# Performance work log

Measured on AMD Instinct MI355X. Metric: run time of the kernel, lower is better.

Reference implementation:

```python
import jax, jax.numpy as jnp
import numpy as np


def setup_inputs() -> dict:
    key = jax.random.key(0)
    ks = jax.random.split(key, 6)
    B, T, D, Dg, U = 64, 2048, 256, 256, 256
    return {
        "x": jax.random.normal(ks[0], (B, T, D), dtype=jnp.float32),
        "g": jax.random.normal(ks[1], (B, 1, Dg), dtype=jnp.float32),
        "W": jax.random.normal(ks[2], (D, U), dtype=jnp.float32) * 0.05,
        "Wg": jax.random.normal(ks[3], (Dg, U), dtype=jnp.float32) * 0.05,
        "b": jax.random.normal(ks[4], (U,), dtype=jnp.float32) * 0.05,
        "v": jax.random.normal(ks[5], (U,), dtype=jnp.float32) * 0.05,
    }


def reference(x, g, W, Wg, b, v):
    # x: [B, T, D], g: [B, 1, Dg]
    g2 = g[:, 0, :]                                  # [B, Dg]
    atten_g = (g2 @ Wg)[:, None, :]                  # [B, 1, U]
    # activation is linear (default activation=None in Keras)
    et = jnp.einsum('btd,du->btu', x, W) + atten_g + b   # [B, T, U]
    scores = jnp.einsum('btu,u->bt', et, v)          # [B, T]
    at = jax.nn.softmax(scores, axis=-1)             # softmax over sequence
    return jnp.einsum('bt,btd->bd', at, x)           # weighted sum pooling
```

## Files before the change

kernel.cpp:

```cpp
#include <hip/hip_runtime.h>

#define B 64
#define T 2048
#define D 256
#define U 256
#define NC 16
#define TC (T / NC)


__global__ __launch_bounds__(256) void k_wv(const float* __restrict__ W,
                                            const float* __restrict__ v,
                                            float* __restrict__ wv) {
    int d = threadIdx.x;
    const float4* Wr = (const float4*)(W + d * U);
    const float4* v4 = (const float4*)v;
    float acc = 0.f;
    #pragma unroll 4
    for (int u = 0; u < U / 4; ++u) {
        float4 w = Wr[u];
        float4 vv = v4[u];
        acc += w.x * vv.x + w.y * vv.y + w.z * vv.z + w.w * vv.w;
    }
    wv[d] = acc;
}

__global__ __launch_bounds__(256) void k_scores(const float* __restrict__ x,
                                                const float* __restrict__ wv,
                                                float* __restrict__ scores) {
    int lane = threadIdx.x & 63;
    int wave = threadIdx.x >> 6;
    long long rowbase = (long long)blockIdx.x * 16 + wave * 4;
    float4 w4 = ((const float4*)wv)[lane];
    #pragma unroll
    for (int i = 0; i < 4; ++i) {
        long long r = rowbase + i;
        float4 xv = ((const float4*)(x + r * D))[lane];
        float s = xv.x * w4.x + xv.y * w4.y + xv.z * w4.z + xv.w * w4.w;
        #pragma unroll
        for (int off = 32; off > 0; off >>= 1)
            s += __shfl_down(s, off, 64);
        if (lane == 0) scores[r] = s;
    }
}

__global__ __launch_bounds__(256) void k_softmax(float* __restrict__ scores) {
    int b = blockIdx.x;
    float* s = scores + (long long)b * T;
    int lane = threadIdx.x & 63, wid = threadIdx.x >> 6;
    float loc[T / 256];
    float mx = -1e30f;
    #pragma unroll
    for (int k = 0; k < T / 256; ++k) {
        loc[k] = s[threadIdx.x + k * 256];
        mx = fmaxf(mx, loc[k]);
    }
    #pragma unroll
    for (int off = 32; off > 0; off >>= 1)
        mx = fmaxf(mx, __shfl_down(mx, off, 64));
    __shared__ float sm[4];
    __shared__ float bc[2];
    if (lane == 0) sm[wid] = mx;
    __syncthreads();
    if (threadIdx.x == 0)
        bc[0] = fmaxf(fmaxf(sm[0], sm[1]), fmaxf(sm[2], sm[3]));
    __syncthreads();
    mx = bc[0];
    float sum = 0.f;
    #pragma unroll
    for (int k = 0; k < T / 256; ++k) {
        loc[k] = __expf(loc[k] - mx);
        sum += loc[k];
    }
    #pragma unroll
    for (int off = 32; off > 0; off >>= 1)
        sum += __shfl_down(sum, off, 64);
    __syncthreads();
    if (lane == 0) sm[wid] = sum;
    __syncthreads();
    if (threadIdx.x == 0)
        bc[1] = 1.f / (sm[0] + sm[1] + sm[2] + sm[3]);
    __syncthreads();
    float inv = bc[1];
    #pragma unroll
    for (int k = 0; k < T / 256; ++k)
        s[threadIdx.x + k * 256] = loc[k] * inv;
}

__global__ __launch_bounds__(256) void k_accum(const float* __restrict__ x,
                                               const float* __restrict__ p,
                                               float* __restrict__ partial) {
    int b = blockIdx.x >> 4;
    int c = blockIdx.x & (NC - 1);
    int l = threadIdx.x & 63;
    int q = threadIdx.x >> 6;
    const float4* xb = (const float4*)(x + ((long long)b * T + (long long)c * TC) * D);
    const float* pb = p + (long long)b * T + c * TC;
    float4 acc = {0.f, 0.f, 0.f, 0.f};
    for (int t = q; t < TC; t += 4) {
        float pv = pb[t];
        float4 xv = xb[(long long)t * 64 + l];
        acc.x = fmaf(pv, xv.x, acc.x);
        acc.y = fmaf(pv, xv.y, acc.y);
        acc.z = fmaf(pv, xv.z, acc.z);
        acc.w = fmaf(pv, xv.w, acc.w);
    }
    __shared__ float4 red[4][64];
    red[q][l] = acc;
    __syncthreads();
    if (q == 0) {
        float4 a0 = red[0][l], a1 = red[1][l], a2 = red[2][l], a3 = red[3][l];
        float4 r;
        r.x = a0.x + a1.x + a2.x + a3.x;
        r.y = a0.y + a1.y + a2.y + a3.y;
        r.z = a0.z + a1.z + a2.z + a3.z;
        r.w = a0.w + a1.w + a2.w + a3.w;
        ((float4*)(partial + (long long)blockIdx.x * D))[l] = r;
    }
}

__global__ __launch_bounds__(256) void k_reduce(const float* __restrict__ partial,
                                               float* __restrict__ out) {
    int b = blockIdx.x;
    int d = threadIdx.x;
    float acc = 0.f;
    #pragma unroll
    for (int c = 0; c < NC; ++c)
        acc += partial[((long long)(b * NC + c)) * D + d];
    out[(long long)b * D + d] = acc;
}

extern "C" void kernel_launch(void* const* d_in, const int* in_sizes, int n_in,
                              void* d_out, int out_size, void* d_ws, size_t ws_size,
                              hipStream_t stream) {
    const float* x = (const float*)d_in[0];
    const float* W = (const float*)d_in[2];
    const float* v = (const float*)d_in[5];
    float* ws = (float*)d_ws;
    float* wv      = ws;
    float* scores  = ws + 256;
    float* partial = ws + 256 + B * T;
    float* out = (float*)d_out;

    k_wv<<<1, 256, 0, stream>>>(W, v, wv);
    k_scores<<<(B * T) / 16, 256, 0, stream>>>(x, wv, scores);
    k_softmax<<<B, 256, 0, stream>>>(scores);
    k_accum<<<B * NC, 256, 0, stream>>>(x, scores, partial);
    k_reduce<<<B, 256, 0, stream>>>(partial, out);
}
```

Baseline: 232.1 us.

## Fuse scores, softmax and pooling into single-pass online-softmax kernel

Replaces the separate score, softmax and weighted-accumulate kernels with one kernel that computes each row's score and keeps a running max, sum and rescaled accumulator (online softmax). Per-chunk partial max, sum and output are combined in a final kernel. This reads x once instead of twice (x is 128 MiB) and removes two launches. In exchange, every row now pays two exps and a serial cross-lane reduction inside the streaming loop, which may limit how much memory traffic stays in flight.

After: 211.2 us. 1.1x faster.

```diff
diff --git a/kernel.cpp b/kernel.cpp
--- a/kernel.cpp
+++ b/kernel.cpp
@@ -7,6 +7,10 @@
 #define NC 16
 #define TC (T / NC)
 
+#define WS_WV   0
+#define WS_M    (WS_WV + 256)
+#define WS_L    (WS_M + B * NC)
+#define WS_O    (WS_L + B * NC)
 
 __global__ __launch_bounds__(256) void k_wv(const float* __restrict__ W,
                                             const float* __restrict__ v,
@@ -24,109 +28,81 @@
     wv[d] = acc;
 }
 
-__global__ __launch_bounds__(256) void k_scores(const float* __restrict__ x,
-                                                const float* __restrict__ wv,
-                                                float* __restrict__ scores) {
-    int lane = threadIdx.x & 63;
-    int wave = threadIdx.x >> 6;
-    long long rowbase = (long long)blockIdx.x * 16 + wave * 4;
-    float4 w4 = ((const float4*)wv)[lane];
-    #pragma unroll
-    for (int i = 0; i < 4; ++i) {
-        long long r = rowbase + i;
-        float4 xv = ((const float4*)(x + r * D))[lane];
-        float s = xv.x * w4.x + xv.y * w4.y + xv.z * w4.z + xv.w * w4.w;
-        #pragma unroll
-        for (int off = 32; off > 0; off >>= 1)
-            s += __shfl_down(s, off, 64);
-        if (lane == 0) scores[r] = s;
-    }
-}
-
-__global__ __launch_bounds__(256) void k_softmax(float* __restrict__ scores) {
-    int b = blockIdx.x;
-    float* s = scores + (long long)b * T;
-    int lane = threadIdx.x & 63, wid = threadIdx.x >> 6;
-    float loc[T / 256];
-    float mx = -1e30f;
-    #pragma unroll
-    for (int k = 0; k < T / 256; ++k) {
-        loc[k] = s[threadIdx.x + k * 256];
-        mx = fmaxf(mx, loc[k]);
-    }
-    #pragma unroll
-    for (int off = 32; off > 0; off >>= 1)
-        mx = fmaxf(mx, __shfl_down(mx, off, 64));
-    __shared__ float sm[4];
-    __shared__ float bc[2];
-    if (lane == 0) sm[wid] = mx;
-    __syncthreads();
-    if (threadIdx.x == 0)
-        bc[0] = fmaxf(fmaxf(sm[0], sm[1]), fmaxf(sm[2], sm[3]));
-    __syncthreads();
-    mx = bc[0];
-    float sum = 0.f;
-    #pragma unroll
-    for (int k = 0; k < T / 256; ++k) {
-        loc[k] = __expf(loc[k] - mx);
-        sum += loc[k];
-    }
-    #pragma unroll
-    for (int off = 32; off > 0; off >>= 1)
-        sum += __shfl_down(sum, off, 64);
-    __syncthreads();
-    if (lane == 0) sm[wid] = sum;
-    __syncthreads();
-    if (threadIdx.x == 0)
-        bc[1] = 1.f / (sm[0] + sm[1] + sm[2] + sm[3]);
-    __syncthreads();
-    float inv = bc[1];
-    #pragma unroll
-    for (int k = 0; k < T / 256; ++k)
-        s[threadIdx.x + k * 256] = loc[k] * inv;
-}
-
-__global__ __launch_bounds__(256) void k_accum(const float* __restrict__ x,
-                                               const float* __restrict__ p,
-                                               float* __restrict__ partial) {
+__global__ __launch_bounds__(256) void k_fused(const float* __restrict__ x,
+                                               const float* __restrict__ wv,
+                                               float* __restrict__ pM,
+                                               float* __restrict__ pL,
+                                               float* __restrict__ pO) {
     int b = blockIdx.x >> 4;
     int c = blockIdx.x & (NC - 1);
     int l = threadIdx.x & 63;
     int q = threadIdx.x >> 6;
-    const float4* xb = (const float4*)(x + ((long long)b * T + (long long)c * TC) * D);
-    const float* pb = p + (long long)b * T + c * TC;
+
+    float4 w4 = ((const float4*)wv)[l];
+    const float4* xb =
+        (const float4*)(x + ((long long)b * T + (long long)c * TC) * D);
+
+    float m = -1e30f, lsum = 0.f;
     float4 acc = {0.f, 0.f, 0.f, 0.f};
+
     for (int t = q; t < TC; t += 4) {
-        float pv = pb[t];
         float4 xv = xb[(long long)t * 64 + l];
-        acc.x = fmaf(pv, xv.x, acc.x);
-        acc.y = fmaf(pv, xv.y, acc.y);
-        acc.z = fmaf(pv, xv.z, acc.z);
-        acc.w = fmaf(pv, xv.w, acc.w);
+        float s = xv.x * w4.x + xv.y * w4.y + xv.z * w4.z + xv.w * w4.w;
+        #pragma unroll
+        for (int off = 1; off < 64; off <<= 1)
+            s += __shfl_xor(s, off, 64);
+        float m_new = fmaxf(m, s);
+        float alpha = __expf(m - m_new);
+        float p = __expf(s - m_new);
+        lsum = lsum * alpha + p;
+        acc.x = fmaf(p, xv.x, acc.x * alpha);
+        acc.y = fmaf(p, xv.y, acc.y * alpha);
+        acc.z = fmaf(p, xv.z, acc.z * alpha);
+        acc.w = fmaf(p, xv.w, acc.w * alpha);
+        m = m_new;
     }
-    __shared__ float4 red[4][64];
-    red[q][l] = acc;
+
+    __shared__ float4 redO[4][64];
+    __shared__ float redM[4], redL[4];
+    redO[q][l] = acc;
+    if (l == 0) { redM[q] = m; redL[q] = lsum; }
     __syncthreads();
     if (q == 0) {
-        float4 a0 = red[0][l], a1 = red[1][l], a2 = red[2][l], a3 = red[3][l];
+        float M = fmaxf(fmaxf(redM[0], redM[1]), fmaxf(redM[2], redM[3]));
+        float e0 = __expf(redM[0] - M), e1 = __expf(redM[1] - M);
+        float e2 = __expf(redM[2] - M), e3 = __expf(redM[3] - M);
+        float4 a0 = redO[0][l], a1 = redO[1][l], a2 = redO[2][l], a3 = redO[3][l];
         float4 r;
-        r.x = a0.x + a1.x + a2.x + a3.x;
-        r.y = a0.y + a1.y + a2.y + a3.y;
-        r.z = a0.z + a1.z + a2.z + a3.z;
-        r.w = a0.w + a1.w + a2.w + a3.w;
-        ((float4*)(partial + (long long)blockIdx.x * D))[l] = r;
+        r.x = a0.x * e0 + a1.x * e1 + a2.x * e2 + a3.x * e3;
+        r.y = a0.y * e0 + a1.y * e1 + a2.y * e2 + a3.y * e3;
+        r.z = a0.z * e0 + a1.z * e1 + a2.z * e2 + a3.z * e3;
+        r.w = a0.w * e0 + a1.w * e1 + a2.w * e2 + a3.w * e3;
+        ((float4*)(pO + (long long)blockIdx.x * D))[l] = r;
+        if (l == 0) {
+            pM[blockIdx.x] = M;
+            pL[blockIdx.x] = redL[0] * e0 + redL[1] * e1 + redL[2] * e2 + redL[3] * e3;
+        }
     }
 }
 
-__global__ __launch_bounds__(256) void k_reduce(const float* __restrict__ partial,
-                                               float* __restrict__ out) {
+__global__ __launch_bounds__(256) void k_combine(const float* __restrict__ pM,
+                                                 const float* __restrict__ pL,
+                                                 const float* __restrict__ pO,
+                                                 float* __restrict__ out) {
     int b = blockIdx.x;
     int d = threadIdx.x;
-    float acc = 0.f;
+    float M = -1e30f;
     #pragma unroll
     for (int c = 0; c < NC; ++c)
-        acc += partial[((long long)(b * NC + c)) * D + d];
-    out[(long long)b * D + d] = acc;
+        M = fmaxf(M, pM[b * NC + c]);
+    float denom = 0.f, acc = 0.f;
+    #pragma unroll
+    for (int c = 0; c < NC; ++c) {
+        float e = __expf(pM[b * NC + c] - M);
+        denom += e * pL[b * NC + c];
+        acc = fmaf(e, pO[((long long)(b * NC + c)) * D + d], acc);
+    }
+    out[(long long)b * D + d] = acc / denom;
 }
 
 extern "C" void kernel_launch(void* const* d_in, const int* in_sizes, int n_in,
@@ -136,14 +112,13 @@
     const float* W = (const float*)d_in[2];
     const float* v = (const float*)d_in[5];
     float* ws = (float*)d_ws;
-    float* wv      = ws;
-    float* scores  = ws + 256;
-    float* partial = ws + 256 + B * T;
+    float* wv = ws + WS_WV;
+    float* pM = ws + WS_M;
+    float* pL = ws + WS_L;
+    float* pO = ws + WS_O;
     float* out = (float*)d_out;
 
     k_wv<<<1, 256, 0, stream>>>(W, v, wv);
-    k_scores<<<(B * T) / 16, 256, 0, stream>>>(x, wv, scores);
-    k_softmax<<<B, 256, 0, stream>>>(scores);
-    k_accum<<<B * NC, 256, 0, stream>>>(x, scores, partial);
-    k_reduce<<<B, 256, 0, stream>>>(partial, out);
+    k_fused<<<B * NC, 256, 0, stream>>>(x, wv, pM, pL, pO);
+    k_combine<<<B, 256, 0, stream>>>(pM, pL, pO, out);
 }
```
